# Kernel optimization log

Measured on AMD Instinct MI355X. Metric: run time of the kernel, lower is better.

Reference implementation:

```python
import jax, jax.numpy as jnp
import numpy as np

B, T_ENC, ENC, DEC, MEL = 32, 1024, 1024, 1024, 80


def setup_inputs() -> dict:
    key = jax.random.key(0)
    ks = jax.random.split(key, 10)
    s = lambda k, shape, sc=1.0: (jax.random.normal(k, shape, dtype=jnp.float32) * sc)
    return {
        "prev_mel_frame": s(ks[0], (B, MEL)),
        "encoder_outputs": s(ks[1], (B, T_ENC, ENC)),
        "h": s(ks[2], (B, DEC)),
        "c": s(ks[3], (B, DEC)),
        # AdditiveAttention learned scale vector (use_scale=True default)
        "attn_scale": s(ks[4], (ENC,), 0.05),
        # LSTMCell params: input dim = MEL + ENC, gates order i, f, c, o (Keras)
        "kernel": s(ks[5], (MEL + ENC, 4 * DEC), 0.02),
        "rec_kernel": s(ks[6], (DEC, 4 * DEC), 0.02),
        "bias": s(ks[7], (4 * DEC,), 0.02),
        # Dense projection to mel
        "proj_w": s(ks[8], (DEC, MEL), 0.02),
        "proj_b": s(ks[9], (MEL,), 0.02),
    }


def reference(prev_mel_frame, encoder_outputs, h, c,
              attn_scale, kernel, rec_kernel, bias, proj_w, proj_b):
    # Additive (Bahdanau) attention: scores[b,t] = sum_d scale_d * tanh(h[b,d] + enc[b,t,d])
    feat = jnp.tanh(h[:, None, :] + encoder_outputs)          # [B, T, D]
    scores = jnp.einsum("btd,d->bt", feat, attn_scale)         # [B, T]
    attn = jax.nn.softmax(scores, axis=-1)
    context = jnp.einsum("bt,btd->bd", attn, encoder_outputs)  # [B, ENC]

    # LSTMCell step on concat([prev_mel, context])
    x = jnp.concatenate([prev_mel_frame, context], axis=-1)    # [B, MEL+ENC]
    z = x @ kernel + h @ rec_kernel + bias                     # [B, 4*DEC]
    i, f, g, o = jnp.split(z, 4, axis=-1)
    i = jax.nn.sigmoid(i)
    f = jax.nn.sigmoid(f)
    o = jax.nn.sigmoid(o)
    c_new = f * c + i * jnp.tanh(g)
    h_new = o * jnp.tanh(c_new)

    mel_frame = h_new @ proj_w + proj_b                        # [B, MEL]
    return mel_frame, h_new, c_new
```

## Files before the change

kernel.cpp:

```cpp
#include <hip/hip_runtime.h>

#define BB 32
#define TT 1024
#define ENCD 1024
#define DECD 1024
#define MELD 80
#define KTOT (MELD + ENCD + DECD)
#define NZ (4 * DECD)
#define KCH 136
#define KC 16
#define NTT 32
#define QR 8

__device__ float g_cp[NTT * BB * ENCD];
__device__ float g_m[NTT * BB];
__device__ float g_s[NTT * BB];
__device__ float g_ctx[BB * ENCD];
__device__ float g_zp[KC * BB * NZ];
__device__ float g_hn[BB * DECD];

__device__ __forceinline__ float tanh_fast(float x) {
    return 1.f - __fdividef(2.f, __expf(2.f * x) + 1.f);
}
__device__ __forceinline__ float sigmoid_fast(float x) {
    return __fdividef(1.f, 1.f + __expf(-x));
}

__global__ __launch_bounds__(256, 4) void k_attn(const float* __restrict__ enc,
                                                 const float* __restrict__ hst,
                                                 const float* __restrict__ scale) {
    __shared__ float es[QR][ENCD];
    __shared__ float ssc[QR];
    int b = blockIdx.x, tc = blockIdx.y;
    int tid = threadIdx.x, w = tid >> 6, lane = tid & 63;
    const float4* hp = (const float4*)(hst + (size_t)b * DECD);
    const float4* sp = (const float4*)scale;
    float4 hr0 = hp[lane], hr1 = hp[lane + 64], hr2 = hp[lane + 128], hr3 = hp[lane + 192];
    float4 sr0 = sp[lane], sr1 = sp[lane + 64], sr2 = sp[lane + 128], sr3 = sp[lane + 192];

    float M = -1e30f, S = 0.f;
    float cx = 0.f, cy = 0.f, cz = 0.f, cw = 0.f;
    const float4* ebase = (const float4*)(enc + ((size_t)b * TT + tc * 32) * ENCD);

    for (int q = 0; q < 4; q++) {
#pragma unroll
        for (int rr = 0; rr < 2; rr++) {
            int r = w * 2 + rr;
            const float4* ep = ebase + (size_t)(q * QR + r) * (ENCD / 4) + lane;
            float4 e0 = ep[0], e1 = ep[64], e2 = ep[128], e3 = ep[192];
            float sc = 0.f;
            sc = fmaf(sr0.x, tanh_fast(hr0.x + e0.x), sc);
            sc = fmaf(sr0.y, tanh_fast(hr0.y + e0.y), sc);
            sc = fmaf(sr0.z, tanh_fast(hr0.z + e0.z), sc);
            sc = fmaf(sr0.w, tanh_fast(hr0.w + e0.w), sc);
            sc = fmaf(sr1.x, tanh_fast(hr1.x + e1.x), sc);
            sc = fmaf(sr1.y, tanh_fast(hr1.y + e1.y), sc);
            sc = fmaf(sr1.z, tanh_fast(hr1.z + e1.z), sc);
            sc = fmaf(sr1.w, tanh_fast(hr1.w + e1.w), sc);
            sc = fmaf(sr2.x, tanh_fast(hr2.x + e2.x), sc);
            sc = fmaf(sr2.y, tanh_fast(hr2.y + e2.y), sc);
            sc = fmaf(sr2.z, tanh_fast(hr2.z + e2.z), sc);
            sc = fmaf(sr2.w, tanh_fast(hr2.w + e2.w), sc);
            sc = fmaf(sr3.x, tanh_fast(hr3.x + e3.x), sc);
            sc = fmaf(sr3.y, tanh_fast(hr3.y + e3.y), sc);
            sc = fmaf(sr3.z, tanh_fast(hr3.z + e3.z), sc);
            sc = fmaf(sr3.w, tanh_fast(hr3.w + e3.w), sc);
#pragma unroll
            for (int off = 32; off; off >>= 1) sc += __shfl_xor(sc, off, 64);
            float4* esr = (float4*)&es[r][0];
            esr[lane] = e0; esr[lane + 64] = e1;
            esr[lane + 128] = e2; esr[lane + 192] = e3;
            if (lane == 0) ssc[r] = sc;
        }
        __syncthreads();
        float s0 = ssc[0], s1 = ssc[1], s2 = ssc[2], s3 = ssc[3];
        float s4 = ssc[4], s5 = ssc[5], s6 = ssc[6], s7 = ssc[7];
        float mq = fmaxf(fmaxf(fmaxf(s0, s1), fmaxf(s2, s3)),
                         fmaxf(fmaxf(s4, s5), fmaxf(s6, s7)));
        float Mn = fmaxf(M, mq);
        float alO = __expf(M - Mn);
        float w0 = __expf(s0 - Mn), w1 = __expf(s1 - Mn);
        float w2 = __expf(s2 - Mn), w3 = __expf(s3 - Mn);
        float w4 = __expf(s4 - Mn), w5 = __expf(s5 - Mn);
        float w6 = __expf(s6 - Mn), w7 = __expf(s7 - Mn);
        float Sq = ((w0 + w1) + (w2 + w3)) + ((w4 + w5) + (w6 + w7));
        S = fmaf(S, alO, Sq);
        M = Mn;
        cx *= alO; cy *= alO; cz *= alO; cw *= alO;
        const float4* col = (const float4*)&es[0][0] + tid;
        float wr[QR] = {w0, w1, w2, w3, w4, w5, w6, w7};
#pragma unroll
        for (int r = 0; r < QR; r++) {
            float4 e = col[r * 256];
            cx = fmaf(wr[r], e.x, cx); cy = fmaf(wr[r], e.y, cy);
            cz = fmaf(wr[r], e.z, cz); cw = fmaf(wr[r], e.w, cw);
        }
        __syncthreads();
    }
    float4 r4; r4.x = cx; r4.y = cy; r4.z = cz; r4.w = cw;
    ((float4*)g_cp)[((size_t)tc * BB + b) * (ENCD / 4) + tid] = r4;
    if (tid == 0) { g_m[tc * BB + b] = M; g_s[tc * BB + b] = S; }
}

__global__ __launch_bounds__(128) void k_combine() {
    __shared__ float wgt[NTT];
    int b = blockIdx.x, dq = blockIdx.y, tid = threadIdx.x;
    float M = -1e30f;
#pragma unroll
    for (int tt = 0; tt < NTT; tt++) M = fmaxf(M, g_m[tt * BB + b]);
    float S = 0.f;
#pragma unroll
    for (int tt = 0; tt < NTT; tt++) S += g_s[tt * BB + b] * __expf(g_m[tt * BB + b] - M);
    if (tid < NTT) wgt[tid] = __expf(g_m[tid * BB + b] - M) * __fdividef(1.f, S);
    __syncthreads();
    int d = dq * 128 + tid;
    float acc = 0.f;
#pragma unroll 8
    for (int tt = 0; tt < NTT; tt++)
        acc = fmaf(wgt[tt], g_cp[((size_t)tt * BB + b) * ENCD + d], acc);
    g_ctx[b * ENCD + d] = acc;
}

__global__ __launch_bounds__(256) void k_zmm(const float* __restrict__ pm,
                                             const float* __restrict__ h,
                                             const float* __restrict__ kern,
                                             const float* __restrict__ reck) {
    __shared__ float xs[KCH * 32];
    __shared__ float sacc[32 * 128];
    int jt = blockIdx.x & 31, kc = blockIdx.x >> 5;
    int k0 = kc * KCH;
    int kcount = min(KCH, KTOT - k0);
    int tid = threadIdx.x;
    for (int idx = tid; idx < kcount * 32; idx += 256) {
        int kk = idx >> 5, b = idx & 31;
        int k = k0 + kk;
        float v;
        if (k < MELD)             v = pm[b * MELD + k];
        else if (k < MELD + ENCD) v = g_ctx[b * ENCD + (k - MELD)];
        else                      v = h[b * DECD + (k - MELD - ENCD)];
        xs[idx] = v;
    }
    __syncthreads();
    int jl = tid & 127, kh = tid >> 7;
    int j = jt * 128 + jl;
    int split = (kcount == KCH) ? 72 : 48;
    int kb = kh ? split : 0;
    int ke = kh ? kcount : split;
    float acc[32];
#pragma unroll
    for (int b = 0; b < 32; b++) acc[b] = 0.f;
    for (int kk0 = kb; kk0 < ke; kk0 += 8) {
        float w[8];
#pragma unroll
        for (int i = 0; i < 8; i++) {
            int k = k0 + kk0 + i;
            w[i] = (k < MELD + ENCD) ? kern[(size_t)k * NZ + j]
                                     : reck[(size_t)(k - MELD - ENCD) * NZ + j];
        }
#pragma unroll
        for (int i = 0; i < 8; i++) {
            const float* xr = xs + (kk0 + i) * 32;
#pragma unroll
            for (int b = 0; b < 32; b++) acc[b] = fmaf(xr[b], w[i], acc[b]);
        }
    }
    if (kh) {
#pragma unroll
        for (int b = 0; b < 32; b++) sacc[b * 128 + jl] = acc[b];
    }
    __syncthreads();
    if (!kh) {
#pragma unroll
        for (int b = 0; b < 32; b++)
            g_zp[((size_t)kc * BB + b) * NZ + j] = acc[b] + sacc[b * 128 + jl];
    }
}

__global__ __launch_bounds__(256) void k_gates(const float* __restrict__ bias,
                                               const float* __restrict__ c,
                                               float* __restrict__ out) {
    __shared__ float sacc[4][4][64];
    int b = blockIdx.x >> 4, jq = blockIdx.x & 15;
    int jl = threadIdx.x & 63, grp = threadIdx.x >> 6;
    int j = jq * 64 + jl;
    int kc0 = grp * 4;
    int kc1 = kc0 + 4;
    float zi = 0.f, zf = 0.f, zg = 0.f, zo = 0.f;
    for (int kc = kc0; kc < kc1; kc++) {
        const float* zp = g_zp + ((size_t)kc * BB + b) * NZ;
        zi += zp[j];
        zf += zp[1024 + j];
        zg += zp[2048 + j];
        zo += zp[3072 + j];
    }
    sacc[grp][0][jl] = zi; sacc[grp][1][jl] = zf;
    sacc[grp][2][jl] = zg; sacc[grp][3][jl] = zo;
    __syncthreads();
    if (grp == 0) {
        zi = sacc[0][0][jl] + sacc[1][0][jl] + sacc[2][0][jl] + sacc[3][0][jl] + bias[j];
        zf = sacc[0][1][jl] + sacc[1][1][jl] + sacc[2][1][jl] + sacc[3][1][jl] + bias[1024 + j];
        zg = sacc[0][2][jl] + sacc[1][2][jl] + sacc[2][2][jl] + sacc[3][2][jl] + bias[2048 + j];
        zo = sacc[0][3][jl] + sacc[1][3][jl] + sacc[2][3][jl] + sacc[3][3][jl] + bias[3072 + j];
        int idx = b * 1024 + j;
        float cn = sigmoid_fast(zf) * c[idx] + sigmoid_fast(zi) * tanh_fast(zg);
        float hn = sigmoid_fast(zo) * tanh_fast(cn);
        g_hn[idx] = hn;
        out[2560 + idx] = hn;
        out[35328 + idx] = cn;
    }
}

__global__ __launch_bounds__(256) void k_proj(const float* __restrict__ pw,
                                              const float* __restrict__ pb,
                                              float* __restrict__ out) {
    __shared__ float lh[1024];
    __shared__ float pacc[2][MELD];
    int b = blockIdx.x, tid = threadIdx.x;
    for (int i = tid; i < 1024; i += 256) lh[i] = g_hn[b * 1024 + i];
    __syncthreads();
    int m = tid & 127;
    int g = tid >> 7;
    if (m < MELD) {
        float acc = 0.f;
        int d0 = g * 512;
#pragma unroll 8
        for (int d = d0; d < d0 + 512; d++) acc = fmaf(lh[d], pw[d * MELD + m], acc);
        pacc[g][m] = acc;
    }
    __syncthreads();
    if (tid < MELD) out[b * MELD + tid] = pacc[0][tid] + pacc[1][tid] + pb[tid];
}

extern "C" void kernel_launch(void* const* d_in, const int* in_sizes, int n_in,
                              void* d_out, int out_size, void* d_ws, size_t ws_size,
                              hipStream_t stream) {
    const float* pm   = (const float*)d_in[0];
    const float* enc  = (const float*)d_in[1];
    const float* h    = (const float*)d_in[2];
    const float* c    = (const float*)d_in[3];
    const float* asc  = (const float*)d_in[4];
    const float* kern = (const float*)d_in[5];
    const float* reck = (const float*)d_in[6];
    const float* bias = (const float*)d_in[7];
    const float* pw   = (const float*)d_in[8];
    const float* pb   = (const float*)d_in[9];
    float* out = (float*)d_out;

    k_attn   <<<dim3(32, NTT), 256, 0, stream>>>(enc, h, asc);
    k_combine<<<dim3(32, 8), 128, 0, stream>>>();
    k_zmm    <<<512, 256, 0, stream>>>(pm, h, kern, reck);
    k_gates  <<<512, 256, 0, stream>>>(bias, c, out);
    k_proj   <<<32, 256, 0, stream>>>(pw, pb, out);
}
```

Baseline: 287.7 us.

## Double-buffer attention rows and fuse softmax combine via last-block atomic

```diff
diff --git a/kernel.cpp b/kernel.cpp
--- a/kernel.cpp
+++ b/kernel.cpp
@@ -10,7 +10,7 @@
 #define KCH 136
 #define KC 16
 #define NTT 32
-#define QR 8
+#define QR 4
 
 __device__ float g_cp[NTT * BB * ENCD];
 __device__ float g_m[NTT * BB];
@@ -18,6 +18,7 @@
 __device__ float g_ctx[BB * ENCD];
 __device__ float g_zp[KC * BB * NZ];
 __device__ float g_hn[BB * DECD];
+__device__ int   g_cnt[BB];
 
 __device__ __forceinline__ float tanh_fast(float x) {
     return 1.f - __fdividef(2.f, __expf(2.f * x) + 1.f);
@@ -29,8 +30,10 @@
 __global__ __launch_bounds__(256, 4) void k_attn(const float* __restrict__ enc,
                                                  const float* __restrict__ hst,
                                                  const float* __restrict__ scale) {
-    __shared__ float es[QR][ENCD];
-    __shared__ float ssc[QR];
+    __shared__ float es[2][QR][ENCD];
+    __shared__ float ssc[2][QR];
+    __shared__ int lastFlag;
+    __shared__ float wgt[NTT];
     int b = blockIdx.x, tc = blockIdx.y;
     int tid = threadIdx.x, w = tid >> 6, lane = tid & 63;
     const float4* hp = (const float4*)(hst + (size_t)b * DECD);
@@ -42,83 +45,94 @@
     float cx = 0.f, cy = 0.f, cz = 0.f, cw = 0.f;
     const float4* ebase = (const float4*)(enc + ((size_t)b * TT + tc * 32) * ENCD);
 
-    for (int q = 0; q < 4; q++) {
-#pragma unroll
-        for (int rr = 0; rr < 2; rr++) {
-            int r = w * 2 + rr;
-            const float4* ep = ebase + (size_t)(q * QR + r) * (ENCD / 4) + lane;
-            float4 e0 = ep[0], e1 = ep[64], e2 = ep[128], e3 = ep[192];
-            float sc = 0.f;
-            sc = fmaf(sr0.x, tanh_fast(hr0.x + e0.x), sc);
-            sc = fmaf(sr0.y, tanh_fast(hr0.y + e0.y), sc);
-            sc = fmaf(sr0.z, tanh_fast(hr0.z + e0.z), sc);
-            sc = fmaf(sr0.w, tanh_fast(hr0.w + e0.w), sc);
-            sc = fmaf(sr1.x, tanh_fast(hr1.x + e1.x), sc);
-            sc = fmaf(sr1.y, tanh_fast(hr1.y + e1.y), sc);
-            sc = fmaf(sr1.z, tanh_fast(hr1.z + e1.z), sc);
-            sc = fmaf(sr1.w, tanh_fast(hr1.w + e1.w), sc);
-            sc = fmaf(sr2.x, tanh_fast(hr2.x + e2.x), sc);
-            sc = fmaf(sr2.y, tanh_fast(hr2.y + e2.y), sc);
-            sc = fmaf(sr2.z, tanh_fast(hr2.z + e2.z), sc);
-            sc = fmaf(sr2.w, tanh_fast(hr2.w + e2.w), sc);
-            sc = fmaf(sr3.x, tanh_fast(hr3.x + e3.x), sc);
-            sc = fmaf(sr3.y, tanh_fast(hr3.y + e3.y), sc);
-            sc = fmaf(sr3.z, tanh_fast(hr3.z + e3.z), sc);
-            sc = fmaf(sr3.w, tanh_fast(hr3.w + e3.w), sc);
-#pragma unroll
-            for (int off = 32; off; off >>= 1) sc += __shfl_xor(sc, off, 64);
-            float4* esr = (float4*)&es[r][0];
-            esr[lane] = e0; esr[lane + 64] = e1;
-            esr[lane + 128] = e2; esr[lane + 192] = e3;
-            if (lane == 0) ssc[r] = sc;
-        }
-        __syncthreads();
-        float s0 = ssc[0], s1 = ssc[1], s2 = ssc[2], s3 = ssc[3];
-        float s4 = ssc[4], s5 = ssc[5], s6 = ssc[6], s7 = ssc[7];
-        float mq = fmaxf(fmaxf(fmaxf(s0, s1), fmaxf(s2, s3)),
-                         fmaxf(fmaxf(s4, s5), fmaxf(s6, s7)));
+    auto stage = [&](int p, int buf) {
+        const float4* ep = ebase + (size_t)(p * QR + w) * (ENCD / 4) + lane;
+        float4 e0 = ep[0], e1 = ep[64], e2 = ep[128], e3 = ep[192];
+        float sc = 0.f;
+        sc = fmaf(sr0.x, tanh_fast(hr0.x + e0.x), sc);
+        sc = fmaf(sr0.y, tanh_fast(hr0.y + e0.y), sc);
+        sc = fmaf(sr0.z, tanh_fast(hr0.z + e0.z), sc);
+        sc = fmaf(sr0.w, tanh_fast(hr0.w + e0.w), sc);
+        sc = fmaf(sr1.x, tanh_fast(hr1.x + e1.x), sc);
+        sc = fmaf(sr1.y, tanh_fast(hr1.y + e1.y), sc);
+        sc = fmaf(sr1.z, tanh_fast(hr1.z + e1.z), sc);
+        sc = fmaf(sr1.w, tanh_fast(hr1.w + e1.w), sc);
+        sc = fmaf(sr2.x, tanh_fast(hr2.x + e2.x), sc);
+        sc = fmaf(sr2.y, tanh_fast(hr2.y + e2.y), sc);
+        sc = fmaf(sr2.z, tanh_fast(hr2.z + e2.z), sc);
+        sc = fmaf(sr2.w, tanh_fast(hr2.w + e2.w), sc);
+        sc = fmaf(sr3.x, tanh_fast(hr3.x + e3.x), sc);
+        sc = fmaf(sr3.y, tanh_fast(hr3.y + e3.y), sc);
+        sc = fmaf(sr3.z, tanh_fast(hr3.z + e3.z), sc);
+        sc = fmaf(sr3.w, tanh_fast(hr3.w + e3.w), sc);
+#pragma unroll
+        for (int off = 32; off; off >>= 1) sc += __shfl_xor(sc, off, 64);
+        float4* esr = (float4*)&es[buf][w][0];
+        esr[lane] = e0; esr[lane + 64] = e1;
+        esr[lane + 128] = e2; esr[lane + 192] = e3;
+        if (lane == 0) ssc[buf][w] = sc;
+    };
+    auto consume = [&](int buf) {
+        float s0 = ssc[buf][0], s1 = ssc[buf][1], s2 = ssc[buf][2], s3 = ssc[buf][3];
+        float mq = fmaxf(fmaxf(s0, s1), fmaxf(s2, s3));
         float Mn = fmaxf(M, mq);
         float alO = __expf(M - Mn);
         float w0 = __expf(s0 - Mn), w1 = __expf(s1 - Mn);
         float w2 = __expf(s2 - Mn), w3 = __expf(s3 - Mn);
-        float w4 = __expf(s4 - Mn), w5 = __expf(s5 - Mn);
-        float w6 = __expf(s6 - Mn), w7 = __expf(s7 - Mn);
-        float Sq = ((w0 + w1) + (w2 + w3)) + ((w4 + w5) + (w6 + w7));
-        S = fmaf(S, alO, Sq);
+        S = fmaf(S, alO, (w0 + w1) + (w2 + w3));
         M = Mn;
         cx *= alO; cy *= alO; cz *= alO; cw *= alO;
-        const float4* col = (const float4*)&es[0][0] + tid;
-        float wr[QR] = {w0, w1, w2, w3, w4, w5, w6, w7};
-#pragma unroll
-        for (int r = 0; r < QR; r++) {
-            float4 e = col[r * 256];
-            cx = fmaf(wr[r], e.x, cx); cy = fmaf(wr[r], e.y, cy);
-            cz = fmaf(wr[r], e.z, cz); cw = fmaf(wr[r], e.w, cw);
-        }
+        const float4* col = (const float4*)&es[buf][0][0] + tid;
+        float4 e;
+        e = col[0];   cx = fmaf(w0, e.x, cx); cy = fmaf(w0, e.y, cy);
+                      cz = fmaf(w0, e.z, cz); cw = fmaf(w0, e.w, cw);
+        e = col[256]; cx = fmaf(w1, e.x, cx); cy = fmaf(w1, e.y, cy);
+                      cz = fmaf(w1, e.z, cz); cw = fmaf(w1, e.w, cw);
+        e = col[512]; cx = fmaf(w2, e.x, cx); cy = fmaf(w2, e.y, cy);
+                      cz = fmaf(w2, e.z, cz); cw = fmaf(w2, e.w, cw);
+        e = col[768]; cx = fmaf(w3, e.x, cx); cy = fmaf(w3, e.y, cy);
+                      cz = fmaf(w3, e.z, cz); cw = fmaf(w3, e.w, cw);
+    };
+
+    stage(0, 0);
+    __syncthreads();
+#pragma unroll
+    for (int p = 0; p < 8; p++) {
+        if (p < 7) stage(p + 1, (p + 1) & 1);
+        consume(p & 1);
         __syncthreads();
     }
+
     float4 r4; r4.x = cx; r4.y = cy; r4.z = cz; r4.w = cw;
     ((float4*)g_cp)[((size_t)tc * BB + b) * (ENCD / 4) + tid] = r4;
     if (tid == 0) { g_m[tc * BB + b] = M; g_s[tc * BB + b] = S; }
-}
-
-__global__ __launch_bounds__(128) void k_combine() {
-    __shared__ float wgt[NTT];
-    int b = blockIdx.x, dq = blockIdx.y, tid = threadIdx.x;
-    float M = -1e30f;
-#pragma unroll
-    for (int tt = 0; tt < NTT; tt++) M = fmaxf(M, g_m[tt * BB + b]);
-    float S = 0.f;
-#pragma unroll
-    for (int tt = 0; tt < NTT; tt++) S += g_s[tt * BB + b] * __expf(g_m[tt * BB + b] - M);
-    if (tid < NTT) wgt[tid] = __expf(g_m[tid * BB + b] - M) * __fdividef(1.f, S);
-    __syncthreads();
-    int d = dq * 128 + tid;
-    float acc = 0.f;
+
+    __threadfence();
+    __syncthreads();
+    if (tid == 0) lastFlag = (atomicAdd(&g_cnt[b], 1) == NTT - 1);
+    __syncthreads();
+    if (!lastFlag) return;
+    if (tid == 0) g_cnt[b] = 0;
+    __threadfence();
+    float Mg = -1e30f;
+#pragma unroll
+    for (int tt = 0; tt < NTT; tt++) Mg = fmaxf(Mg, g_m[tt * BB + b]);
+    float Sg = 0.f;
+#pragma unroll
+    for (int tt = 0; tt < NTT; tt++) Sg += g_s[tt * BB + b] * __expf(g_m[tt * BB + b] - Mg);
+    if (tid < NTT) wgt[tid] = __expf(g_m[tid * BB + b] - Mg) * __fdividef(1.f, Sg);
+    __syncthreads();
+    const float4* cp = (const float4*)g_cp + (size_t)b * (ENCD / 4) + tid;
+    float ax = 0.f, ay = 0.f, az = 0.f, aw = 0.f;
 #pragma unroll 8
-    for (int tt = 0; tt < NTT; tt++)
-        acc = fmaf(wgt[tt], g_cp[((size_t)tt * BB + b) * ENCD + d], acc);
-    g_ctx[b * ENCD + d] = acc;
+    for (int tt = 0; tt < NTT; tt++) {
+        float4 v = cp[(size_t)tt * (BB * ENCD / 4)];
+        float wv = wgt[tt];
+        ax = fmaf(wv, v.x, ax); ay = fmaf(wv, v.y, ay);
+        az = fmaf(wv, v.z, az); aw = fmaf(wv, v.w, aw);
+    }
+    float4 r; r.x = ax; r.y = ay; r.z = az; r.w = aw;
+    ((float4*)g_ctx)[b * (ENCD / 4) + tid] = r;
 }
 
 __global__ __launch_bounds__(256) void k_zmm(const float* __restrict__ pm,
@@ -247,7 +261,6 @@
     float* out = (float*)d_out;
 
     k_attn   <<<dim3(32, NTT), 256, 0, stream>>>(enc, h, asc);
-    k_combine<<<dim3(32, 8), 128, 0, stream>>>();
     k_zmm    <<<512, 256, 0, stream>>>(pm, h, kern, reck);
     k_gates  <<<512, 256, 0, stream>>>(bias, c, out);
     k_proj   <<<32, 256, 0, stream>>>(pw, pb, out);
```

After: 413.1 us. 43.6% more time.
